# Optimization experiments

Hardware: AMD Instinct MI355X
Metric: run time of the kernel (lower is better)

## Reference

```python
import jax, jax.numpy as jnp
import numpy as np
from jax import lax

B = 2; H = 32; W = 32; C = 384
NH = 12; NG = 6; KK = 7; STRIDE = 1; ORF = 2.0
CG = C // NG; HC = C // NH; GH = NH // NG; HID = 4 * C
EPS = 1e-5


def layernorm(x, w, b):
    mu = jnp.mean(x, axis=-1, keepdims=True)
    var = jnp.mean((x - mu) ** 2, axis=-1, keepdims=True)
    return (x - mu) * lax.rsqrt(var + EPS) * w + b


def ref_points(Hk, Wk):
    # normalized reference grid in (-1,1), ordering (y, x) as in _get_ref_points
    ry = ((jnp.arange(Hk, dtype=jnp.float32) + 0.5) / Hk) * 2.0 - 1.0
    rx = ((jnp.arange(Wk, dtype=jnp.float32) + 0.5) / Wk) * 2.0 - 1.0
    return jnp.stack(jnp.meshgrid(ry, rx, indexing='ij'), axis=-1)  # (Hk, Wk, 2)


def grid_sample(img, grid):
    # torch F.grid_sample: bilinear, align_corners=True, padding_mode='zeros'
    # img: (N, Cc, Hi, Wi); grid: (N, ..., 2) with (x, y) in [-1, 1]
    N, Cc, Hi, Wi = img.shape
    out_shape = grid.shape[1:-1]
    g = grid.reshape(N, -1, 2)
    x = (g[..., 0] + 1.0) * 0.5 * (Wi - 1)
    y = (g[..., 1] + 1.0) * 0.5 * (Hi - 1)
    x0 = jnp.floor(x); y0 = jnp.floor(y)
    wx1 = x - x0; wy1 = y - y0
    flat = img.reshape(N, Cc, Hi * Wi)
    M = g.shape[1]
    def gather(ix, iy, wgt):
        valid = (ix >= 0) & (ix <= Wi - 1) & (iy >= 0) & (iy <= Hi - 1)
        idx = (jnp.clip(iy, 0, Hi - 1) * Wi + jnp.clip(ix, 0, Wi - 1)).astype(jnp.int32)
        vals = jnp.take_along_axis(flat, jnp.broadcast_to(idx[:, None, :], (N, Cc, M)), axis=2)
        return vals * (wgt * valid.astype(img.dtype))[:, None, :]
    out = (gather(x0, y0, (1 - wx1) * (1 - wy1))
           + gather(x0 + 1, y0, wx1 * (1 - wy1))
           + gather(x0, y0 + 1, (1 - wx1) * wy1)
           + gather(x0 + 1, y0 + 1, wx1 * wy1))
    return out.reshape((N, Cc) + out_shape)


def setup_inputs() -> dict:
    ks = jax.random.split(jax.random.key(0), 16)
    n = lambda k, s, sc=0.02: jax.random.normal(k, s, jnp.float32) * sc
    return dict(
        x=jax.random.normal(ks[0], (B, H * W, C), jnp.float32),
        norm1_w=jnp.ones((C,), jnp.float32), norm1_b=jnp.zeros((C,), jnp.float32),
        wq=n(ks[1], (C, C)), bq=jnp.zeros((C,), jnp.float32),
        wk=n(ks[2], (C, C)), bk=jnp.zeros((C,), jnp.float32),
        wv=n(ks[3], (C, C)), bv=jnp.zeros((C,), jnp.float32),
        wo=n(ks[4], (C, C)), bo=jnp.zeros((C,), jnp.float32),
        off_dw_w=n(ks[5], (CG, 1, KK, KK)), off_dw_b=jnp.zeros((CG,), jnp.float32),
        off_ln_w=jnp.ones((CG,), jnp.float32), off_ln_b=jnp.zeros((CG,), jnp.float32),
        off_pw_w=n(ks[6], (2, CG)),
        rpe_table=n(ks[7], (NH, 2 * H - 1, 2 * W - 1), 0.01),
        norm2_w=jnp.ones((C,), jnp.float32), norm2_b=jnp.zeros((C,), jnp.float32),
        fc1_w=n(ks[8], (HID, C)), fc1_b=jnp.zeros((HID,), jnp.float32),
        fc2_w=n(ks[9], (C, HID)), fc2_b=jnp.zeros((C,), jnp.float32),
    )


def reference(x, norm1_w, norm1_b, wq, bq, wk, bk, wv, bv, wo, bo,
              off_dw_w, off_dw_b, off_ln_w, off_ln_b, off_pw_w, rpe_table,
              norm2_w, norm2_b, fc1_w, fc1_b, fc2_w, fc2_b):
    Bx, L, Cx = x.shape
    shortcut = x
    xn = layernorm(x, norm1_w, norm1_b)
    xi = xn.reshape(Bx, H, W, Cx).transpose(0, 3, 1, 2)  # (B, C, H, W)

    # proj_q (1x1 conv)
    q = jnp.einsum('bchw,dc->bdhw', xi, wq) + bq[None, :, None, None]

    # offset network on per-group channels
    q_off = q.reshape(Bx * NG, CG, H, W)
    o = lax.conv_general_dilated(q_off, off_dw_w, (STRIDE, STRIDE),
                                 [(KK // 2, KK // 2), (KK // 2, KK // 2)],
                                 dimension_numbers=('NCHW', 'OIHW', 'NCHW'),
                                 feature_group_count=CG) + off_dw_b[None, :, None, None]
    o = layernorm(o.transpose(0, 2, 3, 1), off_ln_w, off_ln_b)  # (Bg, Hk, Wk, CG)
    o = jax.nn.gelu(o, approximate=False)
    offset = jnp.einsum('bhwc,pc->bphw', o, off_pw_w)  # (Bg, 2, Hk, Wk)
    Hk, Wk = offset.shape[2], offset.shape[3]
    ns = Hk * Wk
    orange = jnp.array([1.0 / Hk, 1.0 / Wk], jnp.float32).reshape(1, 2, 1, 1)
    offset = jnp.tanh(offset) * orange * ORF
    offset = offset.transpose(0, 2, 3, 1)  # (Bg, Hk, Wk, 2) (y, x)
    pos = offset + ref_points(Hk, Wk)[None]  # offset_range_factor >= 0 branch

    # deformable sampling of the (normed) feature map
    xs = grid_sample(xi.reshape(Bx * NG, CG, H, W), pos[..., ::-1])  # (Bg, CG, Hk, Wk)
    xs = xs.reshape(Bx, Cx, 1, ns)

    k = (jnp.einsum('bcxn,dc->bdxn', xs, wk) + bk[None, :, None, None]).reshape(Bx * NH, HC, ns)
    v = (jnp.einsum('bcxn,dc->bdxn', xs, wv) + bv[None, :, None, None]).reshape(Bx * NH, HC, ns)
    q_ = q.reshape(Bx * NH, HC, H * W)

    attn = jnp.einsum('bcm,bcn->bmn', q_, k) * (HC ** -0.5)  # (B*NH, HW, ns)

    # continuous relative position bias via grid_sample on rpe_table
    rpe = jnp.broadcast_to(rpe_table[None], (Bx, NH, 2 * H - 1, 2 * W - 1)).reshape(
        Bx * NG, GH, 2 * H - 1, 2 * W - 1)
    qg = ref_points(H, W).reshape(H * W, 2)[None]  # (1, HW, 2)
    disp = (qg[:, :, None, :] - pos.reshape(Bx * NG, ns, 2)[:, None, :, :]) * 0.5  # (Bg, HW, ns, 2)
    bias = grid_sample(rpe, disp[..., ::-1])  # (Bg, GH, HW, ns)
    attn = attn + bias.reshape(Bx * NH, H * W, ns)

    attn = jax.nn.softmax(attn, axis=2)
    out = jnp.einsum('bmn,bcn->bcm', attn, v).reshape(Bx, Cx, H, W)
    y = jnp.einsum('bchw,dc->bdhw', out, wo) + bo[None, :, None, None]
    y = y.transpose(0, 2, 3, 1).reshape(Bx, L, Cx)

    x2 = shortcut + y
    h = layernorm(x2, norm2_w, norm2_b)
    h = jax.nn.gelu(h @ fc1_w.T + fc1_b, approximate=False) @ fc2_w.T + fc2_b
    return x2 + h
```

## Files before the change

### kernel.cpp

```cpp
#include <hip/hip_runtime.h>
#include <math.h>

#define Bc 2
#define Hh 32
#define Ww 32
#define Cc 384
#define NHc 12
#define NGc 6
#define CGc 64
#define HCc 32
#define GHc 2
#define HIDc 1536
#define Lc 1024
#define NSc 1024
#define BGc 12

typedef float f32x4 __attribute__((ext_vector_type(4)));
typedef short bf16x8 __attribute__((ext_vector_type(8)));

__device__ __forceinline__ float gelu_f(float v) {
    return 0.5f * v * (1.f + erff(v * 0.70710678118654752440f));
}

__device__ __forceinline__ unsigned short f2bf(float f) {
    unsigned u = __float_as_uint(f);
    u = (u + 0x7FFF + ((u >> 16) & 1)) >> 16;
    return (unsigned short)u;
}

__device__ __forceinline__ float bf2f(unsigned short u) {
    return __uint_as_float((unsigned)u << 16);
}

__global__ __launch_bounds__(256) void prep_kernel(
    const float* __restrict__ wq, const float* __restrict__ wk,
    const float* __restrict__ wv, const float* __restrict__ wo,
    const float* __restrict__ f1, const float* __restrict__ f2,
    unsigned short* __restrict__ dq, unsigned short* __restrict__ dk,
    unsigned short* __restrict__ dv, unsigned short* __restrict__ d_o,
    unsigned short* __restrict__ d1, unsigned short* __restrict__ d2,
    const float* __restrict__ rpe, unsigned short* __restrict__ tbl,
    const float* __restrict__ x, const float* __restrict__ n1w,
    const float* __restrict__ n1b, unsigned short* __restrict__ xnbf)
{
    int bid = blockIdx.x;
    int tid = threadIdx.x;
    if (bid < 1728) {
        const float* s; unsigned short* d; int base;
        if (bid < 144)       { s = wq; d = dq;  base = bid; }
        else if (bid < 288)  { s = wk; d = dk;  base = bid - 144; }
        else if (bid < 432)  { s = wv; d = dv;  base = bid - 288; }
        else if (bid < 576)  { s = wo; d = d_o; base = bid - 432; }
        else if (bid < 1152) { s = f1; d = d1;  base = bid - 576; }
        else                 { s = f2; d = d2;  base = bid - 1152; }
        int i = base * 1024 + tid * 4;
        float4 v = *(const float4*)(s + i);
        ushort4 u;
        u.x = f2bf(v.x); u.y = f2bf(v.y); u.z = f2bf(v.z); u.w = f2bf(v.w);
        *(ushort4*)(d + i) = u;
    } else if (bid < 1920) {
        int blk = bid - 1728;
        int h = blk >> 4;
        int i = (blk & 15) * 256 + tid;
        unsigned short v = 0;
        if (i < 4095) {
            int row = i / 65, cx = i - row * 65;
            if (cx < 63) v = f2bf(rpe[h * 3969 + row * 63 + cx] * 1.44269504f);
        }
        tbl[(size_t)h * 4096 + i] = v;
    } else {
        __shared__ float l1[4], l2[4];
        int row = (bid - 1920) * 2 + (tid >> 7);
        int t = tid & 127;
        const float* xr = x + (size_t)row * Cc;
        float v0 = xr[t], v1 = xr[t + 128], v2 = xr[t + 256];
        float s = v0 + v1 + v2;
        #pragma unroll
        for (int o = 32; o; o >>= 1) s += __shfl_down(s, o);
        if ((tid & 63) == 0) l1[tid >> 6] = s;
        __syncthreads();
        int rbase = (tid >> 7) * 2;
        float mu = (l1[rbase] + l1[rbase + 1]) * (1.f / Cc);
        float d0 = v0 - mu, d1v = v1 - mu, d2v = v2 - mu;
        float q = d0 * d0 + d1v * d1v + d2v * d2v;
        #pragma unroll
        for (int o = 32; o; o >>= 1) q += __shfl_down(q, o);
        if ((tid & 63) == 0) l2[tid >> 6] = q;
        __syncthreads();
        float rstd = rsqrtf((l2[rbase] + l2[rbase + 1]) * (1.f / Cc) + 1e-5f);
        unsigned short* orow = xnbf + (size_t)row * Cc;
        orow[t]       = f2bf(d0 * rstd * n1w[t]       + n1b[t]);
        orow[t + 128] = f2bf(d1v * rstd * n1w[t + 128] + n1b[t + 128]);
        orow[t + 256] = f2bf(d2v * rstd * n1w[t + 256] + n1b[t + 256]);
    }
}

__global__ __launch_bounds__(128) void ln_kernel(
    const float* __restrict__ x, const float* __restrict__ w,
    const float* __restrict__ b, unsigned short* __restrict__ out)
{
    __shared__ float l1[2], l2[2];
    int row = blockIdx.x;
    int t = threadIdx.x;
    const float* xr = x + (size_t)row * Cc;
    float v0 = xr[t], v1 = xr[t + 128], v2 = xr[t + 256];
    float s = v0 + v1 + v2;
    #pragma unroll
    for (int o = 32; o; o >>= 1) s += __shfl_down(s, o);
    if ((t & 63) == 0) l1[t >> 6] = s;
    __syncthreads();
    float mu = (l1[0] + l1[1]) * (1.f / Cc);
    float d0 = v0 - mu, d1 = v1 - mu, d2 = v2 - mu;
    float q = d0 * d0 + d1 * d1 + d2 * d2;
    #pragma unroll
    for (int o = 32; o; o >>= 1) q += __shfl_down(q, o);
    if ((t & 63) == 0) l2[t >> 6] = q;
    __syncthreads();
    float rstd = rsqrtf((l2[0] + l2[1]) * (1.f / Cc) + 1e-5f);
    unsigned short* orow = out + (size_t)row * Cc;
    orow[t]       = f2bf(d0 * rstd * w[t]       + b[t]);
    orow[t + 128] = f2bf(d1 * rstd * w[t + 128] + b[t + 128]);
    orow[t + 256] = f2bf(d2 * rstd * w[t + 256] + b[t + 256]);
}

template<int EPI>
__global__ __launch_bounds__(256) void mfma_gemm(
    const unsigned short* __restrict__ A, const unsigned short* __restrict__ W,
    const float* __restrict__ bias, const float* __restrict__ res,
    void* __restrict__ out1, void* __restrict__ out2, int M, int N, int K)
{
    int w = threadIdx.x >> 6, l = threadIdx.x & 63;
    int col = l & 15, quad = l >> 4;
    int mb = blockIdx.x * 64 + w * 16;
    int n0 = blockIdx.y * 32;
    const unsigned short* Ap = A + (size_t)(mb + col) * K + quad * 8;
    const unsigned short* Wp0 = W + (size_t)(n0 + col) * K + quad * 8;
    const unsigned short* Wp1 = W + (size_t)(n0 + 16 + col) * K + quad * 8;
    f32x4 acc[2] = {};
    #pragma unroll 4
    for (int k0 = 0; k0 < K; k0 += 32) {
        bf16x8 af = *(const bf16x8*)(Ap + k0);
        bf16x8 w0 = *(const bf16x8*)(Wp0 + k0);
        bf16x8 w1 = *(const bf16x8*)(Wp1 + k0);
        acc[0] = __builtin_amdgcn_mfma_f32_16x16x32_bf16(af, w0, acc[0], 0, 0, 0);
        acc[1] = __builtin_amdgcn_mfma_f32_16x16x32_bf16(af, w1, acc[1], 0, 0, 0);
    }
    int bb = mb >> 10, l0 = (mb & 1023) + quad * 4;
    #pragma unroll
    for (int ch = 0; ch < 2; ch++) {
        int n = n0 + ch * 16 + col;
        float bv = bias[n];
        if (EPI == 3) {
            unsigned short u0 = f2bf(acc[ch][0] + bv);
            unsigned short u1 = f2bf(acc[ch][1] + bv);
            unsigned short u2 = f2bf(acc[ch][2] + bv);
            unsigned short u3 = f2bf(acc[ch][3] + bv);
            ushort4 qv = {u0, u1, u2, u3};
            *(ushort4*)&((unsigned short*)out1)[((size_t)(bb * Cc + n)) * Lc + l0] = qv;
            unsigned short* q2 = (unsigned short*)out2;
            size_t base = (((size_t)(bb * NHc + (n >> 5))) * Lc + l0) * 32 + (n & 31);
            q2[base] = u0; q2[base + 32] = u1; q2[base + 64] = u2; q2[base + 96] = u3;
        } else {
            #pragma unroll
            for (int r = 0; r < 4; r++) {
                size_t m = mb + quad * 4 + r;
                float v = acc[ch][r] + bv;
                if (EPI == 1)
                    ((unsigned short*)out1)[m * N + n] = f2bf(gelu_f(v));
                else
                    ((float*)out1)[m * N + n] = v + res[m * N + n];
            }
        }
    }
}

__global__ __launch_bounds__(256) void mfma_kv(
    const unsigned short* __restrict__ A, const unsigned short* __restrict__ Wk,
    const unsigned short* __restrict__ Wv, const float* __restrict__ bk,
    const float* __restrict__ bv, unsigned short* __restrict__ kout,
    unsigned short* __restrict__ vout, int M, int K)
{
    int w = threadIdx.x >> 6, l = threadIdx.x & 63;
    int col = l & 15, quad = l >> 4;
    int mb = blockIdx.x * 64 + w * 16;
    int n0 = blockIdx.y * 32;
    const unsigned short* Ap = A + (size_t)(mb + col) * K + quad * 8;
    const unsigned short* Wk0 = Wk + (size_t)(n0 + col) * K + quad * 8;
    const unsigned short* Wk1 = Wk + (size_t)(n0 + 16 + col) * K + quad * 8;
    const unsigned short* Wv0 = Wv + (size_t)(n0 + col) * K + quad * 8;
    const unsigned short* Wv1 = Wv + (size_t)(n0 + 16 + col) * K + quad * 8;
    f32x4 ak[2] = {}, av[2] = {};
    #pragma unroll 4
    for (int k0 = 0; k0 < K; k0 += 32) {
        bf16x8 af = *(const bf16x8*)(Ap + k0);
        bf16x8 k0f = *(const bf16x8*)(Wk0 + k0);
        bf16x8 k1f = *(const bf16x8*)(Wk1 + k0);
        bf16x8 v0f = *(const bf16x8*)(Wv0 + k0);
        bf16x8 v1f = *(const bf16x8*)(Wv1 + k0);
        ak[0] = __builtin_amdgcn_mfma_f32_16x16x32_bf16(af, k0f, ak[0], 0, 0, 0);
        ak[1] = __builtin_amdgcn_mfma_f32_16x16x32_bf16(af, k1f, ak[1], 0, 0, 0);
        av[0] = __builtin_amdgcn_mfma_f32_16x16x32_bf16(af, v0f, av[0], 0, 0, 0);
        av[1] = __builtin_amdgcn_mfma_f32_16x16x32_bf16(af, v1f, av[1], 0, 0, 0);
    }
    int bb = mb >> 10, l0 = (mb & 1023) + quad * 4;
    #pragma unroll
    for (int ch = 0; ch < 2; ch++) {
        int n = n0 + ch * 16 + col;
        float bkv = bk[n], bvv = bv[n];
        #pragma unroll
        for (int r = 0; r < 4; r++)
            kout[(size_t)(mb + quad * 4 + r) * Cc + n] = f2bf(ak[ch][r] + bkv);
        ushort4 u;
        u.x = f2bf(av[ch][0] + bvv); u.y = f2bf(av[ch][1] + bvv);
        u.z = f2bf(av[ch][2] + bvv); u.w = f2bf(av[ch][3] + bvv);
        *(ushort4*)&vout[((size_t)(bb * Cc + n)) * NSc + l0] = u;
    }
}

__global__ __launch_bounds__(256) void dwconv_kernel(
    const unsigned short* __restrict__ q, const float* __restrict__ wdw,
    const float* __restrict__ bdw, float* __restrict__ o_dw)
{
    int cg = blockIdx.x, bg = blockIdx.y;
    int b = bg / NGc, g = bg % NGc;
    __shared__ float wk_s[49];
    __shared__ float img[1024];
    const unsigned short* qp = q + (size_t)(b * Cc + g * CGc + cg) * Lc;
    if (threadIdx.x < 49) wk_s[threadIdx.x] = wdw[cg * 49 + threadIdx.x];
    #pragma unroll
    for (int i = 0; i < 4; i++)
        img[threadIdx.x + i * 256] = bf2f(qp[threadIdx.x + i * 256]);
    __syncthreads();
    float bias = bdw[cg];
    #pragma unroll
    for (int i = 0; i < 4; i++) {
        int hw = threadIdx.x + i * 256;
        int y = hw >> 5, xx = hw & 31;
        float acc = bias;
        #pragma unroll
        for (int ky = 0; ky < 7; ky++) {
            int yy = y + ky - 3;
            if (yy < 0 || yy > 31) continue;
            #pragma unroll
            for (int kx = 0; kx < 7; kx++) {
                int x2 = xx + kx - 3;
                if (x2 < 0 || x2 > 31) continue;
                acc += img[yy * 32 + x2] * wk_s[ky * 7 + kx];
            }
        }
        o_dw[(size_t)(bg * CGc + cg) * Lc + hw] = acc;
    }
}

__global__ __launch_bounds__(256) void offsample_kernel(
    const float* __restrict__ o_dw, const float* __restrict__ lnw,
    const float* __restrict__ lnb, const float* __restrict__ pw,
    const unsigned short* __restrict__ xn, float* __restrict__ pos,
    unsigned short* __restrict__ xs)
{
    int hw = blockIdx.x * 4 + (threadIdx.x >> 6);
    int bg = blockIdx.y;
    int cg = threadIdx.x & 63;
    int b = bg / NGc, g = bg % NGc;
    float v = o_dw[(size_t)(bg * CGc + cg) * Lc + hw];
    float s = v;
    #pragma unroll
    for (int o = 32; o; o >>= 1) s += __shfl_down(s, o);
    s = __shfl(s, 0, 64);
    float mu = s * (1.f / CGc);
    float d = v - mu;
    float q2 = d * d;
    #pragma unroll
    for (int o = 32; o; o >>= 1) q2 += __shfl_down(q2, o);
    q2 = __shfl(q2, 0, 64);
    float rstd = rsqrtf(q2 * (1.f / CGc) + 1e-5f);
    float t = d * rstd * lnw[cg] + lnb[cg];
    float gl = gelu_f(t);
    float sy = gl * pw[cg];
    float sx = gl * pw[CGc + cg];
    #pragma unroll
    for (int o = 32; o; o >>= 1) {
        sy += __shfl_down(sy, o);
        sx += __shfl_down(sx, o);
    }
    sy = __shfl(sy, 0, 64);
    sx = __shfl(sx, 0, 64);
    int y = hw >> 5, xx = hw & 31;
    float py = tanhf(sy) * 0.0625f + ((y + 0.5f) * (2.f / Hh) - 1.f);
    float px = tanhf(sx) * 0.0625f + ((xx + 0.5f) * (2.f / Ww) - 1.f);
    if (cg == 0) {
        pos[((size_t)bg * Lc + hw) * 2 + 0] = py;
        pos[((size_t)bg * Lc + hw) * 2 + 1] = px;
    }
    float fx = (px + 1.f) * 0.5f * 31.f;
    float fy = (py + 1.f) * 0.5f * 31.f;
    float x0f = floorf(fx), y0f = floorf(fy);
    int x0 = (int)x0f, y0 = (int)y0f;
    float wx1 = fx - x0f, wy1 = fy - y0f;
    float wx0 = 1.f - wx1, wy0 = 1.f - wy1;
    const unsigned short* base = xn + (size_t)(b * Lc) * Cc + g * CGc + cg;
    float acc = 0.f;
    if (y0 >= 0 && y0 <= 31) {
        if (x0 >= 0 && x0 <= 31) acc += bf2f(base[(size_t)(y0 * 32 + x0) * Cc]) * wx0 * wy0;
        if (x0 + 1 >= 0 && x0 + 1 <= 31) acc += bf2f(base[(size_t)(y0 * 32 + x0 + 1) * Cc]) * wx1 * wy0;
    }
    if (y0 + 1 >= 0 && y0 + 1 <= 31) {
        if (x0 >= 0 && x0 <= 31) acc += bf2f(base[(size_t)((y0 + 1) * 32 + x0) * Cc]) * wx0 * wy1;
        if (x0 + 1 >= 0 && x0 + 1 <= 31) acc += bf2f(base[(size_t)((y0 + 1) * 32 + x0 + 1) * Cc]) * wx1 * wy1;
    }
    xs[((size_t)(b * NSc) + hw) * Cc + g * CGc + cg] = f2bf(acc);
}

__global__ __launch_bounds__(256) void attn_kernel(
    const unsigned short* __restrict__ qbf, const unsigned short* __restrict__ kbf,
    const unsigned short* __restrict__ vtb, const float* __restrict__ pos,
    const unsigned short* __restrict__ rpet, unsigned short* __restrict__ attno)
{
    __shared__ float o_smem[2112];
    __shared__ unsigned short p_bf[4][16 * 72];
    __shared__ float l_s[4][16];
    unsigned short* rpe_s = (unsigned short*)o_smem;

    int m0 = blockIdx.x * 16;
    int h = blockIdx.y, b = blockIdx.z;
    int tid = threadIdx.x;
    int w = tid >> 6, l = tid & 63;
    int col = l & 15, quad = l >> 4;

    {
        const unsigned short* tbh = rpet + (size_t)h * 4096;
        #pragma unroll
        for (int i = 0; i < 4; i++) {
            int idx = (tid + i * 256) * 4;
            *(ushort4*)(rpe_s + idx) = *(const ushort4*)(tbh + idx);
        }
    }

    bf16x8 qfrag = *(const bf16x8*)(qbf +
        ((((size_t)(b * NHc + h)) * Lc + m0 + col) * 32 + quad * 8));

    float qgy = ((m0 >> 5) + 0.5f) * (2.f / 32.f) - 1.f;
    float qgx0 = (((m0 & 31) + quad * 4) + 0.5f) * (2.f / 32.f) - 1.f;

    const unsigned short* kb_ = kbf + (size_t)b * NSc * Cc + h * HCc;
    const unsigned short* vb_ = vtb + ((size_t)(b * Cc + h * HCc)) * NSc;
    const float2* pp = (const float2*)(pos + (size_t)(b * NGc + (h >> 1)) * NSc * 2);

    float run_l[4] = {0.f, 0.f, 0.f, 0.f};
    f32x4 O0 = {0.f, 0.f, 0.f, 0.f};
    f32x4 O1 = {0.f, 0.f, 0.f, 0.f};

    __syncthreads();

    for (int it = 0; it < 4; it++) {
        int n0 = w * 256 + it * 64;
        f32x4 s[4];
        #pragma unroll
        for (int ch = 0; ch < 4; ch++) {
            bf16x8 kf = *(const bf16x8*)(kb_ +
                ((size_t)(n0 + ch * 16 + col) * Cc + quad * 8));
            f32x4 z = {0.f, 0.f, 0.f, 0.f};
            s[ch] = __builtin_amdgcn_mfma_f32_16x16x32_bf16(qfrag, kf, z, 0, 0, 0);
        }
        #pragma unroll
        for (int ch = 0; ch < 4; ch++) {
            int n = n0 + ch * 16 + col;
            float2 pyx = pp[n];
            float fy = ((qgy - pyx.x) * 0.5f + 1.f) * 31.f;
            float y0f = floorf(fy);
            int iy = (int)y0f;
            float wy1 = fy - y0f, wy0 = 1.f - wy1;
            bool y0ok = (unsigned)iy <= 62u;
            bool y1ok = (unsigned)(iy + 1) <= 62u;
            const unsigned short* r0 = rpe_s + iy * 65;
            float fx0 = ((qgx0 - pyx.y) * 0.5f + 1.f) * 31.f;
            #pragma unroll
            for (int r = 0; r < 4; r++) {
                float fx = fx0 + r * 0.96875f;
                float x0f = floorf(fx);
                int ix = (int)x0f;
                float wx1 = fx - x0f, wx0 = 1.f - wx1;
                bool x0ok = (unsigned)ix <= 62u;
                bool x1ok = (unsigned)(ix + 1) <= 62u;
                float bias = 0.f;
                if (y0ok) {
                    if (x0ok) bias += bf2f(r0[ix]) * wy0 * wx0;
                    if (x1ok) bias += bf2f(r0[ix + 1]) * wy0 * wx1;
                }
                if (y1ok) {
                    if (x0ok) bias += bf2f(r0[65 + ix]) * wy1 * wx0;
                    if (x1ok) bias += bf2f(r0[65 + ix + 1]) * wy1 * wx1;
                }
                s[ch][r] = s[ch][r] * 0.25506974f + bias;
            }
        }
        float rowsum[4] = {0.f, 0.f, 0.f, 0.f};
        #pragma unroll
        for (int ch = 0; ch < 4; ch++)
            #pragma unroll
            for (int r = 0; r < 4; r++) {
                float e = exp2f(s[ch][r]);
                s[ch][r] = e;
                rowsum[r] += e;
            }
        #pragma unroll
        for (int r = 0; r < 4; r++) run_l[r] += rowsum[r];
        #pragma unroll
        for (int ch = 0; ch < 4; ch++)
            #pragma unroll
            for (int r = 0; r < 4; r++)
                p_bf[w][(quad * 4 + r) * 72 + ch * 16 + col] = f2bf(s[ch][r]);
        #pragma unroll
        for (int half = 0; half < 2; half++) {
            bf16x8 pf = *(const bf16x8*)&p_bf[w][col * 72 + half * 32 + quad * 8];
            bf16x8 v0 = *(const bf16x8*)(vb_ +
                ((size_t)col * NSc + n0 + half * 32 + quad * 8));
            O0 = __builtin_amdgcn_mfma_f32_16x16x32_bf16(pf, v0, O0, 0, 0, 0);
            bf16x8 v1 = *(const bf16x8*)(vb_ +
                ((size_t)(col + 16) * NSc + n0 + half * 32 + quad * 8));
            O1 = __builtin_amdgcn_mfma_f32_16x16x32_bf16(pf, v1, O1, 0, 0, 0);
        }
    }
    #pragma unroll
    for (int r = 0; r < 4; r++) {
        float sm = run_l[r];
        #pragma unroll
        for (int msk = 1; msk < 16; msk <<= 1)
            sm += __shfl_xor(sm, msk);
        run_l[r] = sm;
    }
    __syncthreads();
    float* o_s = o_smem;
    #pragma unroll
    for (int r = 0; r < 4; r++) {
        int m = quad * 4 + r;
        o_s[w * 528 + m * 33 + col] = O0[r];
        o_s[w * 528 + m * 33 + col + 16] = O1[r];
    }
    if (col == 0) {
        #pragma unroll
        for (int r = 0; r < 4; r++)
            l_s[w][quad * 4 + r] = run_l[r];
    }
    __syncthreads();
    for (int i = tid; i < 512; i += 256) {
        int m = i >> 5, c = i & 31;
        float lsum = l_s[0][m] + l_s[1][m] + l_s[2][m] + l_s[3][m];
        float osum = o_s[0 * 528 + m * 33 + c] + o_s[1 * 528 + m * 33 + c]
                   + o_s[2 * 528 + m * 33 + c] + o_s[3 * 528 + m * 33 + c];
        attno[((size_t)(b * Lc) + m0 + m) * Cc + h * HCc + c] = f2bf(osum / lsum);
    }
}

extern "C" void kernel_launch(void* const* d_in, const int* in_sizes, int n_in,
                              void* d_out, int out_size, void* d_ws, size_t ws_size,
                              hipStream_t stream)
{
    const float* x    = (const float*)d_in[0];
    const float* n1w  = (const float*)d_in[1];
    const float* n1b  = (const float*)d_in[2];
    const float* wq   = (const float*)d_in[3];
    const float* bq   = (const float*)d_in[4];
    const float* wk   = (const float*)d_in[5];
    const float* bk   = (const float*)d_in[6];
    const float* wv   = (const float*)d_in[7];
    const float* bv   = (const float*)d_in[8];
    const float* wo   = (const float*)d_in[9];
    const float* bo   = (const float*)d_in[10];
    const float* dw_w = (const float*)d_in[11];
    const float* dw_b = (const float*)d_in[12];
    const float* lnw  = (const float*)d_in[13];
    const float* lnb  = (const float*)d_in[14];
    const float* pw_w = (const float*)d_in[15];
    const float* rpe  = (const float*)d_in[16];
    const float* n2w  = (const float*)d_in[17];
    const float* n2b  = (const float*)d_in[18];
    const float* fc1w = (const float*)d_in[19];
    const float* fc1b = (const float*)d_in[20];
    const float* fc2w = (const float*)d_in[21];
    const float* fc2b = (const float*)d_in[22];
    float* out = (float*)d_out;

    float* ws = (float*)d_ws;
    unsigned short* xnbf = (unsigned short*)ws;
    unsigned short* qb16 = (unsigned short*)(ws + 393216);
    unsigned short* qbf  = (unsigned short*)(ws + 1179648);
    unsigned short* h1bf = (unsigned short*)ws;
    float* odw   = ws + 1572864;
    unsigned short* xln2bf = (unsigned short*)(ws + 1572864);
    float* posb  = ws + 2359296;
    unsigned short* xsbf = (unsigned short*)(ws + 2383872);
    unsigned short* kbf  = (unsigned short*)(ws + 2777088);
    unsigned short* vtb  = (unsigned short*)(ws + 3170304);
    unsigned short* attnbf = (unsigned short*)(ws + 3563520);
    float* x2    = ws + 3956736;
    unsigned short* wqbf   = (unsigned short*)(ws + 4743168);
    unsigned short* wkbf   = (unsigned short*)(ws + 4816896);
    unsigned short* wvbf   = (unsigned short*)(ws + 4890624);
    unsigned short* wobf   = (unsigned short*)(ws + 4964352);
    unsigned short* fc1wbf = (unsigned short*)(ws + 5038080);
    unsigned short* fc2wbf = (unsigned short*)(ws + 5332992);
    unsigned short* rpet   = (unsigned short*)(ws + 5627904);

    prep_kernel<<<2944, 256, 0, stream>>>(
        wq, wk, wv, wo, fc1w, fc2w, wqbf, wkbf, wvbf, wobf, fc1wbf, fc2wbf,
        rpe, rpet, x, n1w, n1b, xnbf);
    mfma_gemm<3><<<dim3(Bc * Lc / 64, Cc / 32), 256, 0, stream>>>(
        xnbf, wqbf, bq, x, qb16, qbf, Bc * Lc, Cc, Cc);
    dwconv_kernel<<<dim3(CGc, BGc), 256, 0, stream>>>(qb16, dw_w, dw_b, odw);
    offsample_kernel<<<dim3(Lc / 4, BGc), 256, 0, stream>>>(
        odw, lnw, lnb, pw_w, xnbf, posb, xsbf);
    mfma_kv<<<dim3(Bc * NSc / 64, Cc / 32), 256, 0, stream>>>(
        xsbf, wkbf, wvbf, bk, bv, kbf, vtb, Bc * NSc, Cc);
    attn_kernel<<<dim3(Lc / 16, NHc, Bc), 256, 0, stream>>>(
        qbf, kbf, vtb, posb, rpet, attnbf);
    mfma_gemm<2><<<dim3(Bc * Lc / 64, Cc / 32), 256, 0, stream>>>(
        attnbf, wobf, bo, x, x2, x2, Bc * Lc, Cc, Cc);
    ln_kernel<<<Bc * Lc, 128, 0, stream>>>(x2, n2w, n2b, xln2bf);
    mfma_gemm<1><<<dim3(Bc * Lc / 64, HIDc / 32), 256, 0, stream>>>(
        xln2bf, fc1wbf, fc1b, x2, h1bf, h1bf, Bc * Lc, HIDc, Cc);
    mfma_gemm<2><<<dim3(Bc * Lc / 64, Cc / 32), 256, 0, stream>>>(
        h1bf, fc2wbf, fc2b, x2, out, out, Bc * Lc, Cc, HIDc);
}
```

Baseline: 274.7 us.

## Split attention key range across two blocks with separate merge kernel

Splits each attention tile's 1024 keys into two halves handled by separate blocks, doubling the grid, and writes partial unnormalized outputs and row sums to workspace. A new merge kernel sums the two partials and normalizes before writing bf16 output. The aim is more parallelism and occupancy for the attention stage. The cost is an extra launch, fp32 partial traffic, and a per-block fixed overhead (rpe table load, q fragment) that is now paid twice.

```diff
diff --git a/kernel.cpp b/kernel.cpp
--- a/kernel.cpp
+++ b/kernel.cpp
@@ -314,7 +314,8 @@
 __global__ __launch_bounds__(256) void attn_kernel(
     const unsigned short* __restrict__ qbf, const unsigned short* __restrict__ kbf,
     const unsigned short* __restrict__ vtb, const float* __restrict__ pos,
-    const unsigned short* __restrict__ rpet, unsigned short* __restrict__ attno)
+    const unsigned short* __restrict__ rpet, float* __restrict__ pO,
+    float* __restrict__ pL)
 {
     __shared__ float o_smem[2112];
     __shared__ unsigned short p_bf[4][16 * 72];
@@ -322,7 +323,8 @@
     unsigned short* rpe_s = (unsigned short*)o_smem;
 
     int m0 = blockIdx.x * 16;
-    int h = blockIdx.y, b = blockIdx.z;
+    int h = blockIdx.y >> 1, half = blockIdx.y & 1;
+    int b = blockIdx.z;
     int tid = threadIdx.x;
     int w = tid >> 6, l = tid & 63;
     int col = l & 15, quad = l >> 4;
@@ -352,8 +354,8 @@
 
     __syncthreads();
 
-    for (int it = 0; it < 4; it++) {
-        int n0 = w * 256 + it * 64;
+    for (int it = 0; it < 2; it++) {
+        int n0 = half * 512 + w * 128 + it * 64;
         f32x4 s[4];
         #pragma unroll
         for (int ch = 0; ch < 4; ch++) {
@@ -411,13 +413,13 @@
             for (int r = 0; r < 4; r++)
                 p_bf[w][(quad * 4 + r) * 72 + ch * 16 + col] = f2bf(s[ch][r]);
         #pragma unroll
-        for (int half = 0; half < 2; half++) {
-            bf16x8 pf = *(const bf16x8*)&p_bf[w][col * 72 + half * 32 + quad * 8];
+        for (int hn = 0; hn < 2; hn++) {
+            bf16x8 pf = *(const bf16x8*)&p_bf[w][col * 72 + hn * 32 + quad * 8];
             bf16x8 v0 = *(const bf16x8*)(vb_ +
-                ((size_t)col * NSc + n0 + half * 32 + quad * 8));
+                ((size_t)col * NSc + n0 + hn * 32 + quad * 8));
             O0 = __builtin_amdgcn_mfma_f32_16x16x32_bf16(pf, v0, O0, 0, 0, 0);
             bf16x8 v1 = *(const bf16x8*)(vb_ +
-                ((size_t)(col + 16) * NSc + n0 + half * 32 + quad * 8));
+                ((size_t)(col + 16) * NSc + n0 + hn * 32 + quad * 8));
             O1 = __builtin_amdgcn_mfma_f32_16x16x32_bf16(pf, v1, O1, 0, 0, 0);
         }
     }
@@ -443,12 +445,29 @@
             l_s[w][quad * 4 + r] = run_l[r];
     }
     __syncthreads();
+    size_t tile = (((size_t)(b * NHc + h) * 64) + blockIdx.x) * 2 + half;
     for (int i = tid; i < 512; i += 256) {
         int m = i >> 5, c = i & 31;
-        float lsum = l_s[0][m] + l_s[1][m] + l_s[2][m] + l_s[3][m];
         float osum = o_s[0 * 528 + m * 33 + c] + o_s[1 * 528 + m * 33 + c]
                    + o_s[2 * 528 + m * 33 + c] + o_s[3 * 528 + m * 33 + c];
-        attno[((size_t)(b * Lc) + m0 + m) * Cc + h * HCc + c] = f2bf(osum / lsum);
+        pO[tile * 512 + i] = osum;
+        if (c == 0)
+            pL[tile * 16 + m] = l_s[0][m] + l_s[1][m] + l_s[2][m] + l_s[3][m];
+    }
+}
+
+__global__ __launch_bounds__(256) void attn_merge(
+    const float* __restrict__ pO, const float* __restrict__ pL,
+    unsigned short* __restrict__ attno)
+{
+    int mt = blockIdx.x, h = blockIdx.y, b = blockIdx.z;
+    size_t tile0 = (((size_t)(b * NHc + h) * 64) + mt) * 2;
+    int tid = threadIdx.x;
+    for (int i = tid; i < 512; i += 256) {
+        int m = i >> 5, c = i & 31;
+        float lsum = pL[tile0 * 16 + m] + pL[(tile0 + 1) * 16 + m];
+        float o = pO[tile0 * 512 + i] + pO[(tile0 + 1) * 512 + i];
+        attno[((size_t)(b * Lc) + mt * 16 + m) * Cc + h * HCc + c] = f2bf(o / lsum);
     }
 }
 
@@ -486,21 +505,23 @@
     unsigned short* qb16 = (unsigned short*)(ws + 393216);
     unsigned short* qbf  = (unsigned short*)(ws + 1179648);
     unsigned short* h1bf = (unsigned short*)ws;
-    float* odw   = ws + 1572864;
-    unsigned short* xln2bf = (unsigned short*)(ws + 1572864);
-    float* posb  = ws + 2359296;
-    unsigned short* xsbf = (unsigned short*)(ws + 2383872);
-    unsigned short* kbf  = (unsigned short*)(ws + 2777088);
-    unsigned short* vtb  = (unsigned short*)(ws + 3170304);
-    unsigned short* attnbf = (unsigned short*)(ws + 3563520);
-    float* x2    = ws + 3956736;
-    unsigned short* wqbf   = (unsigned short*)(ws + 4743168);
-    unsigned short* wkbf   = (unsigned short*)(ws + 4816896);
-    unsigned short* wvbf   = (unsigned short*)(ws + 4890624);
-    unsigned short* wobf   = (unsigned short*)(ws + 4964352);
-    unsigned short* fc1wbf = (unsigned short*)(ws + 5038080);
-    unsigned short* fc2wbf = (unsigned short*)(ws + 5332992);
-    unsigned short* rpet   = (unsigned short*)(ws + 5627904);
+    float* pO    = ws;
+    float* pL    = ws + 1572864;
+    float* odw   = ws + 1671168;
+    unsigned short* xln2bf = (unsigned short*)(ws + 1671168);
+    float* posb  = ws + 2457600;
+    unsigned short* xsbf = (unsigned short*)(ws + 2482176);
+    unsigned short* kbf  = (unsigned short*)(ws + 2875392);
+    unsigned short* vtb  = (unsigned short*)(ws + 3268608);
+    unsigned short* attnbf = (unsigned short*)(ws + 3661824);
+    float* x2    = ws + 4055040;
+    unsigned short* wqbf   = (unsigned short*)(ws + 4841472);
+    unsigned short* wkbf   = (unsigned short*)(ws + 4915200);
+    unsigned short* wvbf   = (unsigned short*)(ws + 4988928);
+    unsigned short* wobf   = (unsigned short*)(ws + 5062656);
+    unsigned short* fc1wbf = (unsigned short*)(ws + 5136384);
+    unsigned short* fc2wbf = (unsigned short*)(ws + 5431296);
+    unsigned short* rpet   = (unsigned short*)(ws + 5726208);
 
     prep_kernel<<<2944, 256, 0, stream>>>(
         wq, wk, wv, wo, fc1w, fc2w, wqbf, wkbf, wvbf, wobf, fc1wbf, fc2wbf,
@@ -512,8 +533,9 @@
         odw, lnw, lnb, pw_w, xnbf, posb, xsbf);
     mfma_kv<<<dim3(Bc * NSc / 64, Cc / 32), 256, 0, stream>>>(
         xsbf, wkbf, wvbf, bk, bv, kbf, vtb, Bc * NSc, Cc);
-    attn_kernel<<<dim3(Lc / 16, NHc, Bc), 256, 0, stream>>>(
-        qbf, kbf, vtb, posb, rpet, attnbf);
+    attn_kernel<<<dim3(Lc / 16, NHc * 2, Bc), 256, 0, stream>>>(
+        qbf, kbf, vtb, posb, rpet, pO, pL);
+    attn_merge<<<dim3(Lc / 16, NHc, Bc), 256, 0, stream>>>(pO, pL, attnbf);
     mfma_gemm<2><<<dim3(Bc * Lc / 64, Cc / 32), 256, 0, stream>>>(
         attnbf, wobf, bo, x, x2, x2, Bc * Lc, Cc, Cc);
     ln_kernel<<<Bc * Lc, 128, 0, stream>>>(x2, n2w, n2b, xln2bf);
```

After: 274.7 us. Within noise of the previous version (+0.0%).
